# Kernel tuning notes

Measured on AMD Instinct MI355X. Metric: run time of the kernel, lower is better.

Reference implementation:

```python
import jax, jax.numpy as jnp
import numpy as np

N_STREAMS = 8
D_MODEL = 2048
S_EXP = 2
NS = N_STREAMS * S_EXP            # 16
N_SKEW = NS * (NS - 1) // 2       # 120
B, L = 2, 4096

# static upper-triangular index pairs (constants)
_TRIU_R, _TRIU_C = np.triu_indices(NS, k=1)
TRIU_R = jnp.asarray(_TRIU_R)
TRIU_C = jnp.asarray(_TRIU_C)


def setup_inputs() -> dict:
    key = jax.random.key(0)
    k1, k2, k3 = jax.random.split(key, 3)
    streams = jax.random.normal(k1, (B, L, N_STREAMS, D_MODEL), dtype=jnp.float32)
    # W_res: torch Linear weight layout [out_features, in_features]; small init
    # (the module zero-inits, but we use random weights for a meaningful test)
    W = jax.random.normal(k2, (N_SKEW, D_MODEL), dtype=jnp.float32) * 0.02
    b = jax.random.normal(k3, (N_SKEW,), dtype=jnp.float32) * 0.02
    return {"streams": streams, "W": W, "b": b}


def reference(streams, W, b):
    # streams: [B, L, n, d]
    x_agg = streams.mean(axis=2)                      # [B, L, d]
    z = jnp.einsum('bld,kd->blk', x_agg, W) + b       # [B, L, n_skew]
    # build skew-symmetric A: upper triangle = z, lower = -z
    Bq, Lq = z.shape[0], z.shape[1]
    S = jnp.zeros((Bq, Lq, NS, NS), dtype=z.dtype).at[..., TRIU_R, TRIU_C].set(z)
    A = S - jnp.swapaxes(S, -1, -2)                   # [B, L, ns, ns]
    I = jnp.eye(NS, dtype=z.dtype)
    # Cayley transform: Q = (I + A)^{-1} (I - A)  in SO(ns)
    Q = jnp.linalg.solve(I + A, I - A)                # [B, L, ns, ns]
    # block Frobenius norms -> exactly doubly stochastic H_res
    Qb = Q.reshape(Bq, Lq, N_STREAMS, S_EXP, N_STREAMS, S_EXP)
    H_res = (Qb ** 2).sum(axis=(3, 5)) / S_EXP        # [B, L, n, n]
    return H_res
```

## Files before the change

kernel.cpp:

```cpp
#include <hip/hip_runtime.h>

#define NSTR 8
#define DM 2048
#define NK 120
#define NKP 128


__global__ __launch_bounds__(256)
void mean8(const float4* __restrict__ s4, float4* __restrict__ xa4, int pbase) {
    const int t = threadIdx.x;
    const size_t p = blockIdx.x;
    const float4* src = s4 + (size_t)(pbase + p) * (NSTR * DM / 4);
    float4 a = src[t];
    float4 b = src[t + 256];
#pragma unroll
    for (int n = 1; n < 8; ++n) {
        const float4 u = src[(size_t)n * (DM / 4) + t];
        const float4 w = src[(size_t)n * (DM / 4) + t + 256];
        a.x += u.x; a.y += u.y; a.z += u.z; a.w += u.w;
        b.x += w.x; b.y += w.y; b.z += w.z; b.w += w.w;
    }
    a.x *= 0.125f; a.y *= 0.125f; a.z *= 0.125f; a.w *= 0.125f;
    b.x *= 0.125f; b.y *= 0.125f; b.z *= 0.125f; b.w *= 0.125f;
    xa4[p * (DM / 4) + t] = a;
    xa4[p * (DM / 4) + t + 256] = b;
}

__global__ __launch_bounds__(256, 2)
void proj(const float* __restrict__ xa, const float* __restrict__ Wm,
          float* __restrict__ zp, int npos) {
    __shared__ float4 sxa[128 * 16];
    __shared__ float4 sw[128 * 16];

    const int t = threadIdx.x;
    const int slice = blockIdx.x & 7;
    const int ptile = blockIdx.x >> 3;
    const int pos0 = ptile * 128;
    const int typ = t >> 4;
    const int txk = t & 15;
    const int c = t & 15;
    const int rbase = t >> 4;

    float4 ra[8], rw[8];
    float acc[8][8];
#pragma unroll
    for (int i = 0; i < 8; ++i)
#pragma unroll
        for (int j = 0; j < 8; ++j) acc[i][j] = 0.f;

    {
        const int ds0 = slice * 256;
#pragma unroll
        for (int r = 0; r < 8; ++r) {
            const int p = rbase + 16 * r;
            ra[r] = *(const float4*)(xa + (size_t)(pos0 + p) * DM + ds0 + c * 4);
        }
#pragma unroll
        for (int r = 0; r < 8; ++r) {
            const int k = rbase + 16 * r;
            rw[r] = (k < NK) ? *(const float4*)(Wm + (size_t)k * DM + ds0 + c * 4)
                             : make_float4(0.f, 0.f, 0.f, 0.f);
        }
    }

#pragma unroll 1
    for (int sub = 0; sub < 4; ++sub) {
#pragma unroll
        for (int r = 0; r < 8; ++r) {
            const int p = rbase + 16 * r;
            sxa[p * 16 + (c ^ (p >> 3))] = ra[r];
        }
#pragma unroll
        for (int r = 0; r < 8; ++r) {
            const int k = rbase + 16 * r;
            sw[k * 16 + (c ^ (k >> 3))] = rw[r];
        }
        __syncthreads();

        if (sub < 3) {
            const int ds0 = slice * 256 + (sub + 1) * 64;
#pragma unroll
            for (int r = 0; r < 8; ++r) {
                const int p = rbase + 16 * r;
                ra[r] = *(const float4*)(xa + (size_t)(pos0 + p) * DM + ds0 + c * 4);
            }
#pragma unroll
            for (int r = 0; r < 8; ++r) {
                const int k = rbase + 16 * r;
                rw[r] = (k < NK) ? *(const float4*)(Wm + (size_t)k * DM + ds0 + c * 4)
                                 : make_float4(0.f, 0.f, 0.f, 0.f);
            }
        }

        for (int dq = 0; dq < 16; ++dq) {
            float4 a[8];
#pragma unroll
            for (int i = 0; i < 8; ++i) a[i] = sxa[(typ * 8 + i) * 16 + (dq ^ typ)];
#pragma unroll
            for (int j = 0; j < 8; ++j) {
                const float4 bv = sw[(txk * 8 + j) * 16 + (dq ^ txk)];
#pragma unroll
                for (int i = 0; i < 8; ++i) {
                    acc[i][j] = fmaf(a[i].x, bv.x, acc[i][j]);
                    acc[i][j] = fmaf(a[i].y, bv.y, acc[i][j]);
                    acc[i][j] = fmaf(a[i].z, bv.z, acc[i][j]);
                    acc[i][j] = fmaf(a[i].w, bv.w, acc[i][j]);
                }
            }
        }
        __syncthreads();
    }

#pragma unroll
    for (int i = 0; i < 8; ++i) {
        float* dst = zp + ((size_t)(pos0 + typ * 8 + i) * 8 + slice) * NKP + txk * 8;
        *(float4*)dst = make_float4(acc[i][0], acc[i][1], acc[i][2], acc[i][3]);
        *((float4*)dst + 1) = make_float4(acc[i][4], acc[i][5], acc[i][6], acc[i][7]);
    }
}

template <int NPARTS>
__global__ __launch_bounds__(256)
void cayley_k(const float* __restrict__ zp, const float* __restrict__ bvec,
              float* __restrict__ out, int pbase) {
    __shared__ float zrow[4][NKP];
    const int t = threadIdx.x;
    const int wave = t >> 6;
    const int l = t & 63;
    const int pos = blockIdx.x * 4 + wave;
    const int j = l & 15;
    const int g = l >> 4;

    {
        const float4* src = (const float4*)(zp + (size_t)pos * NPARTS * NKP);
        float4 s = make_float4(0.f, 0.f, 0.f, 0.f);
#pragma unroll
        for (int q = 0; q < (NPARTS + 1) / 2; ++q) {
            const int idx = l + 64 * q;
            if (idx < NPARTS * 32) {
                const float4 v = src[idx];
                s.x += v.x; s.y += v.y; s.z += v.z; s.w += v.w;
            }
        }
        s.x += __shfl_xor(s.x, 32, 64);
        s.y += __shfl_xor(s.y, 32, 64);
        s.z += __shfl_xor(s.z, 32, 64);
        s.w += __shfl_xor(s.w, 32, 64);
        if (l < 32) {
            if (l < 30) {
                const float4 b4 = ((const float4*)bvec)[l];
                s.x += b4.x; s.y += b4.y; s.z += b4.z; s.w += b4.w;
            }
            ((float4*)&zrow[wave][0])[l] = s;
        }
    }
    __syncthreads();

    float m[4], x[4];
#pragma unroll
    for (int r = 0; r < 4; ++r) {
        const int i = 4 * r + g;
        float a;
        if (i < j) {
            a = zrow[wave][(i * (31 - i)) / 2 + (j - i - 1)];
        } else if (i > j) {
            a = -zrow[wave][(j * (31 - j)) / 2 + (i - j - 1)];
        } else {
            a = 0.f;
        }
        const float d = (i == j) ? 1.f : 0.f;
        m[r] = d + a;
        x[r] = d - a;
    }

#pragma unroll
    for (int k = 0; k < 16; ++k) {
        const int rr = k >> 2;
        const int src_row = (k & 3) << 4;
        const float mk  = __shfl(m[rr], src_row | j, 64);
        const float xk  = __shfl(x[rr], src_row | j, 64);
        const float mkk = __shfl(m[rr], src_row | k, 64);
        const float rk = 1.0f / mkk;
#pragma unroll
        for (int r = 0; r < 4; ++r) {
            const float mik = __shfl(m[r], (g << 4) | k, 64);
            const float f = (4 * r + g == k) ? 0.f : mik * rk;
            m[r] = fmaf(-f, mk, m[r]);
            x[r] = fmaf(-f, xk, x[r]);
        }
    }

    float h[4];
#pragma unroll
    for (int r = 0; r < 4; ++r) {
        const int i = 4 * r + g;
        const float mdiag = __shfl(m[r], (g << 4) | i, 64);
        const float q = x[r] / mdiag;
        float s = q * q;
        s += __shfl_xor(s, 1, 64);
        s += __shfl_xor(s, 16, 64);
        h[r] = s * 0.5f;
    }
    if (((j & 1) == 0) && ((g & 1) == 0)) {
        const int col = j >> 1;
#pragma unroll
        for (int r = 0; r < 4; ++r) {
            const int row = 2 * r + (g >> 1);
            out[(size_t)(pbase + pos) * 64 + row * 8 + col] = h[r];
        }
    }
}

#define TM 128
#define DSLICE 256
#define SD 64

__global__ void zero_ws(float4* z4) {
    z4[(size_t)blockIdx.x * 256 + threadIdx.x] = make_float4(0.f, 0.f, 0.f, 0.f);
}

__global__ __launch_bounds__(256, 2)
void mean_proj_fused(const float* __restrict__ streams, const float* __restrict__ W,
                     float* __restrict__ z) {
    __shared__ float4 sxa[TM * 16];
    __shared__ float4 sw[NKP * 16];

    const int t = threadIdx.x;
    const int bid = blockIdx.x;
    const int slice = bid >> 6;
    const int ptile = bid & 63;
    const int pos0 = ptile * TM;
    const int typ = t >> 4;
    const int txk = t & 15;

    float acc[8][8];
#pragma unroll
    for (int i = 0; i < 8; ++i)
#pragma unroll
        for (int j = 0; j < 8; ++j) acc[i][j] = 0.f;

    for (int sub = 0; sub < 4; ++sub) {
        const int ds0 = slice * DSLICE + sub * SD;
#pragma unroll
        for (int r = 0; r < 8; ++r) {
            const int item = t + 256 * r;
            const int p = item >> 4;
            const int dq = item & 15;
            const float4* src = (const float4*)(streams
                + (size_t)(pos0 + p) * NSTR * DM + ds0 + dq * 4);
            float4 v = src[0];
#pragma unroll
            for (int n = 1; n < 8; ++n) {
                const float4 u = src[n * (DM / 4)];
                v.x += u.x; v.y += u.y; v.z += u.z; v.w += u.w;
            }
            v.x *= 0.125f; v.y *= 0.125f; v.z *= 0.125f; v.w *= 0.125f;
            sxa[p * 16 + (dq ^ (p >> 3))] = v;
        }
#pragma unroll
        for (int r = 0; r < 8; ++r) {
            const int item = t + 256 * r;
            const int k = item >> 4;
            const int dq = item & 15;
            float4 v = make_float4(0.f, 0.f, 0.f, 0.f);
            if (k < NK) v = *(const float4*)(W + (size_t)k * DM + ds0 + dq * 4);
            sw[k * 16 + (dq ^ (k >> 3))] = v;
        }
        __syncthreads();

        for (int dq = 0; dq < 16; ++dq) {
            float4 a[8];
#pragma unroll
            for (int i = 0; i < 8; ++i) a[i] = sxa[(typ * 8 + i) * 16 + (dq ^ typ)];
#pragma unroll
            for (int j = 0; j < 8; ++j) {
                const float4 bv = sw[(txk * 8 + j) * 16 + (dq ^ txk)];
#pragma unroll
                for (int i = 0; i < 8; ++i) {
                    acc[i][j] = fmaf(a[i].x, bv.x, acc[i][j]);
                    acc[i][j] = fmaf(a[i].y, bv.y, acc[i][j]);
                    acc[i][j] = fmaf(a[i].z, bv.z, acc[i][j]);
                    acc[i][j] = fmaf(a[i].w, bv.w, acc[i][j]);
                }
            }
        }
        __syncthreads();
    }

#pragma unroll
    for (int i = 0; i < 8; ++i) {
        const size_t p = (size_t)pos0 + typ * 8 + i;
#pragma unroll
        for (int j = 0; j < 8; ++j) {
            const int k = txk * 8 + j;
            if (k < NK) atomicAdd(&z[p * NKP + k], acc[i][j]);
        }
    }
}

extern "C" void kernel_launch(void* const* d_in, const int* in_sizes, int n_in,
                              void* d_out, int out_size, void* d_ws, size_t ws_size,
                              hipStream_t stream) {
    const float* streams = (const float*)d_in[0];
    const float* W       = (const float*)d_in[1];
    const float* bvec    = (const float*)d_in[2];
    float* out = (float*)d_out;

    const size_t TOTPOS = 8192;
    const size_t XA_FULL = TOTPOS * DM * sizeof(float);
    const size_t ZP_FULL = 8 * TOTPOS * NKP * sizeof(float);

    int nb = 0;
    size_t npos = 0;
    if (ws_size >= XA_FULL + ZP_FULL)               { nb = 1; npos = 8192; }
    else if (ws_size >= (XA_FULL + ZP_FULL) / 2)    { nb = 2; npos = 4096; }

    if (nb > 0) {
        float* xa = (float*)d_ws;
        float* zp = (float*)((char*)d_ws + npos * DM * sizeof(float));
        for (int b = 0; b < nb; ++b) {
            const int pbase = (int)(b * npos);
            mean8<<<(int)npos, 256, 0, stream>>>(
                (const float4*)streams, (float4*)xa, pbase);
            proj<<<(int)((npos / 128) * 8), 256, 0, stream>>>(xa, W, zp, (int)npos);
            cayley_k<8><<<(int)(npos / 4), 256, 0, stream>>>(zp, bvec, out, pbase);
        }
    } else {
        float* z = (float*)d_ws;
        zero_ws<<<1024, 256, 0, stream>>>((float4*)d_ws);
        mean_proj_fused<<<512, 256, 0, stream>>>(streams, W, z);
        cayley_k<1><<<2048, 256, 0, stream>>>(z, bvec, out, 0);
    }
}
```

Baseline: 780.8 us.

## Double-buffer LDS tiles in projection GEMM and batch loads in mean kernel

The projection kernel now uses two LDS buffers with half-width 32-column k-steps, so the next tile is prefetched into registers and written to the alternate buffer while the current one is computed. This drops one barrier per iteration and halves the staging registers, and the loop runs twice as many k-steps. The mean kernel issues all 16 float4 loads up front and sums them as a tree, which exposes more memory-level parallelism. The risks are a new XOR swizzle that could cause LDS bank conflicts and the extra loop overhead.

Result: slower. 1.398 ms (+79.1%).

```diff
diff --git a/kernel.cpp b/kernel.cpp
--- a/kernel.cpp
+++ b/kernel.cpp
@@ -10,27 +10,35 @@
 void mean8(const float4* __restrict__ s4, float4* __restrict__ xa4, int pbase) {
     const int t = threadIdx.x;
     const size_t p = blockIdx.x;
-    const float4* src = s4 + (size_t)(pbase + p) * (NSTR * DM / 4);
-    float4 a = src[t];
-    float4 b = src[t + 256];
-#pragma unroll
-    for (int n = 1; n < 8; ++n) {
-        const float4 u = src[(size_t)n * (DM / 4) + t];
-        const float4 w = src[(size_t)n * (DM / 4) + t + 256];
-        a.x += u.x; a.y += u.y; a.z += u.z; a.w += u.w;
-        b.x += w.x; b.y += w.y; b.z += w.z; b.w += w.w;
-    }
-    a.x *= 0.125f; a.y *= 0.125f; a.z *= 0.125f; a.w *= 0.125f;
-    b.x *= 0.125f; b.y *= 0.125f; b.z *= 0.125f; b.w *= 0.125f;
-    xa4[p * (DM / 4) + t] = a;
-    xa4[p * (DM / 4) + t + 256] = b;
+    const float4* src = s4 + (size_t)(pbase + p) * (NSTR * DM / 4) + t;
+    float4 u[8], w[8];
+#pragma unroll
+    for (int n = 0; n < 8; ++n) u[n] = src[(size_t)n * (DM / 4)];
+#pragma unroll
+    for (int n = 0; n < 8; ++n) w[n] = src[(size_t)n * (DM / 4) + 256];
+#pragma unroll
+    for (int n = 0; n < 4; ++n) {
+        u[n].x += u[n + 4].x; u[n].y += u[n + 4].y; u[n].z += u[n + 4].z; u[n].w += u[n + 4].w;
+        w[n].x += w[n + 4].x; w[n].y += w[n + 4].y; w[n].z += w[n + 4].z; w[n].w += w[n + 4].w;
+    }
+#pragma unroll
+    for (int n = 0; n < 2; ++n) {
+        u[n].x += u[n + 2].x; u[n].y += u[n + 2].y; u[n].z += u[n + 2].z; u[n].w += u[n + 2].w;
+        w[n].x += w[n + 2].x; w[n].y += w[n + 2].y; w[n].z += w[n + 2].z; w[n].w += w[n + 2].w;
+    }
+    u[0].x += u[1].x; u[0].y += u[1].y; u[0].z += u[1].z; u[0].w += u[1].w;
+    w[0].x += w[1].x; w[0].y += w[1].y; w[0].z += w[1].z; w[0].w += w[1].w;
+    u[0].x *= 0.125f; u[0].y *= 0.125f; u[0].z *= 0.125f; u[0].w *= 0.125f;
+    w[0].x *= 0.125f; w[0].y *= 0.125f; w[0].z *= 0.125f; w[0].w *= 0.125f;
+    xa4[p * (DM / 4) + t] = u[0];
+    xa4[p * (DM / 4) + t + 256] = w[0];
 }
 
 __global__ __launch_bounds__(256, 2)
 void proj(const float* __restrict__ xa, const float* __restrict__ Wm,
           float* __restrict__ zp, int npos) {
-    __shared__ float4 sxa[128 * 16];
-    __shared__ float4 sw[128 * 16];
+    __shared__ float4 sxa[2][128 * 8];
+    __shared__ float4 sw[2][128 * 8];
 
     const int t = threadIdx.x;
     const int slice = blockIdx.x & 7;
@@ -38,67 +46,54 @@
     const int pos0 = ptile * 128;
     const int typ = t >> 4;
     const int txk = t & 15;
-    const int c = t & 15;
-    const int rbase = t >> 4;
-
-    float4 ra[8], rw[8];
+    const int srow = t >> 3;
+    const int sc = t & 7;
+
+    float4 ra[4], rw[4];
     float acc[8][8];
 #pragma unroll
     for (int i = 0; i < 8; ++i)
 #pragma unroll
         for (int j = 0; j < 8; ++j) acc[i][j] = 0.f;
 
-    {
-        const int ds0 = slice * 256;
-#pragma unroll
-        for (int r = 0; r < 8; ++r) {
-            const int p = rbase + 16 * r;
-            ra[r] = *(const float4*)(xa + (size_t)(pos0 + p) * DM + ds0 + c * 4);
-        }
-#pragma unroll
-        for (int r = 0; r < 8; ++r) {
-            const int k = rbase + 16 * r;
-            rw[r] = (k < NK) ? *(const float4*)(Wm + (size_t)k * DM + ds0 + c * 4)
-                             : make_float4(0.f, 0.f, 0.f, 0.f);
-        }
-    }
+    auto loadr = [&](int sub) {
+        const int d0 = slice * 256 + sub * 32 + sc * 4;
+#pragma unroll
+        for (int r = 0; r < 4; ++r) {
+            const int row = srow + 32 * r;
+            ra[r] = *(const float4*)(xa + (size_t)(pos0 + row) * DM + d0);
+            rw[r] = (row < NK) ? *(const float4*)(Wm + (size_t)row * DM + d0)
+                               : make_float4(0.f, 0.f, 0.f, 0.f);
+        }
+    };
+    auto writeb = [&](int buf) {
+#pragma unroll
+        for (int r = 0; r < 4; ++r) {
+            const int row = srow + 32 * r;
+            const int cc = sc ^ (((srow >> 3) + 4 * r) & 7);
+            sxa[buf][row * 8 + cc] = ra[r];
+            sw[buf][row * 8 + cc] = rw[r];
+        }
+    };
+
+    loadr(0);
+    writeb(0);
+    int cur = 0;
 
 #pragma unroll 1
-    for (int sub = 0; sub < 4; ++sub) {
-#pragma unroll
-        for (int r = 0; r < 8; ++r) {
-            const int p = rbase + 16 * r;
-            sxa[p * 16 + (c ^ (p >> 3))] = ra[r];
-        }
-#pragma unroll
-        for (int r = 0; r < 8; ++r) {
-            const int k = rbase + 16 * r;
-            sw[k * 16 + (c ^ (k >> 3))] = rw[r];
-        }
+    for (int sub = 0; sub < 8; ++sub) {
         __syncthreads();
-
-        if (sub < 3) {
-            const int ds0 = slice * 256 + (sub + 1) * 64;
-#pragma unroll
-            for (int r = 0; r < 8; ++r) {
-                const int p = rbase + 16 * r;
-                ra[r] = *(const float4*)(xa + (size_t)(pos0 + p) * DM + ds0 + c * 4);
-            }
-#pragma unroll
-            for (int r = 0; r < 8; ++r) {
-                const int k = rbase + 16 * r;
-                rw[r] = (k < NK) ? *(const float4*)(Wm + (size_t)k * DM + ds0 + c * 4)
-                                 : make_float4(0.f, 0.f, 0.f, 0.f);
-            }
-        }
-
-        for (int dq = 0; dq < 16; ++dq) {
+        if (sub < 7) loadr(sub + 1);
+
+#pragma unroll
+        for (int dq = 0; dq < 8; ++dq) {
             float4 a[8];
 #pragma unroll
-            for (int i = 0; i < 8; ++i) a[i] = sxa[(typ * 8 + i) * 16 + (dq ^ typ)];
+            for (int i = 0; i < 8; ++i)
+                a[i] = sxa[cur][(typ * 8 + i) * 8 + (dq ^ (typ & 7))];
 #pragma unroll
             for (int j = 0; j < 8; ++j) {
-                const float4 bv = sw[(txk * 8 + j) * 16 + (dq ^ txk)];
+                const float4 bv = sw[cur][(txk * 8 + j) * 8 + (dq ^ (txk & 7))];
 #pragma unroll
                 for (int i = 0; i < 8; ++i) {
                     acc[i][j] = fmaf(a[i].x, bv.x, acc[i][j]);
@@ -108,7 +103,9 @@
                 }
             }
         }
-        __syncthreads();
+
+        if (sub < 7) writeb(cur ^ 1);
+        cur ^= 1;
     }
 
 #pragma unroll
```
